# Kernel tuning notes

Hardware: AMD Instinct MI355X
Metric: run time of the kernel (lower is better)

Reference implementation:

```python
import jax, jax.numpy as jnp
import numpy as np

B, S, DIM = 2, 2048, 1024
H, W = 16, 256
HD = DIM // H
SCALE = HD ** -0.5


def setup_inputs() -> dict:
    key = jax.random.key(0)
    ks = jax.random.split(key, 9)
    std = DIM ** -0.5
    return {
        "x": jax.random.normal(ks[0], (B, S, DIM), dtype=jnp.float32),
        "Wq": jax.random.normal(ks[1], (DIM, DIM), dtype=jnp.float32) * std,
        "bq": jnp.zeros((DIM,), dtype=jnp.float32),
        "Wk": jax.random.normal(ks[2], (DIM, DIM), dtype=jnp.float32) * std,
        "bk": jnp.zeros((DIM,), dtype=jnp.float32),
        "Wv": jax.random.normal(ks[3], (DIM, DIM), dtype=jnp.float32) * std,
        "bv": jnp.zeros((DIM,), dtype=jnp.float32),
        "Wo": jax.random.normal(ks[4], (DIM, DIM), dtype=jnp.float32) * std,
        "bo": jnp.zeros((DIM,), dtype=jnp.float32),
    }


def reference(x, Wq, bq, Wk, bk, Wv, bv, Wo, bo):
    b, s, dim = x.shape
    q = (x @ Wq + bq).reshape(b, s, H, HD).transpose(0, 2, 1, 3)  # [B,H,S,HD]
    k = (x @ Wk + bk).reshape(b, s, H, HD).transpose(0, 2, 1, 3)
    v = (x @ Wv + bv).reshape(b, s, H, HD).transpose(0, 2, 1, 3)

    scores = jnp.einsum("bhid,bhjd->bhij", q, k) * SCALE  # [B,H,S,S]
    i = jnp.arange(s)[:, None]
    j = jnp.arange(s)[None, :]
    # valid keys: within causal sliding window [i-W+1, i]
    valid = (j <= i) & (j >= i - W + 1)
    scores = jnp.where(valid, scores, -jnp.inf)
    attn = jax.nn.softmax(scores, axis=-1)
    out = jnp.einsum("bhij,bhjd->bhid", attn, v)  # [B,H,S,HD]
    out = out.transpose(0, 2, 1, 3).reshape(b, s, dim)
    return out @ Wo + bo
```

## Files before the change

### kernel.cpp

```cpp
#include <hip/hip_runtime.h>
#include <stdint.h>

typedef __bf16 bf16;
typedef __bf16 bf16x8 __attribute__((ext_vector_type(8)));
typedef float f32x4 __attribute__((ext_vector_type(4)));

#define MFMA16(a, b, c) __builtin_amdgcn_mfma_f32_16x16x32_bf16((a), (b), (c), 0, 0, 0)

__device__ __forceinline__ void ldsdma16(const void* g, void* l) {
  __builtin_amdgcn_global_load_lds((const __attribute__((address_space(1))) void*)g,
                                   (__attribute__((address_space(3))) void*)l, 16, 0, 0);
}

__global__ __launch_bounds__(256) void prep_kernel(const float* __restrict__ x,
                                                   const float* __restrict__ Wq,
                                                   const float* __restrict__ Wk,
                                                   const float* __restrict__ Wv,
                                                   const float* __restrict__ Wo,
                                                   bf16* __restrict__ WT,
                                                   bf16* __restrict__ xb) {
  if (blockIdx.z == 4) {
    const int t = (blockIdx.y * 16 + blockIdx.x) * 256 + threadIdx.x;
#pragma unroll
    for (int it = 0; it < 16; ++it) {
      const int idx = (it * 65536 + t) * 4;
      float4 v = *(const float4*)(x + idx);
      union { bf16 h[4]; uint2 u; } p;
      p.h[0] = (bf16)v.x; p.h[1] = (bf16)v.y; p.h[2] = (bf16)v.z; p.h[3] = (bf16)v.w;
      *(uint2*)(xb + idx) = p.u;
    }
    return;
  }
  __shared__ float tile[64][65];
  const float* src = blockIdx.z == 0 ? Wq : blockIdx.z == 1 ? Wk : blockIdx.z == 2 ? Wv : Wo;
  bf16* dst = WT + (size_t)blockIdx.z * 1024 * 1024;
  const int k0 = blockIdx.y * 64, n0 = blockIdx.x * 64;
  const int rr = threadIdx.x >> 6, c = threadIdx.x & 63;
#pragma unroll
  for (int i = 0; i < 16; ++i) {
    int r = i * 4 + rr;
    tile[r][c] = src[(size_t)(k0 + r) * 1024 + n0 + c];
  }
  __syncthreads();
#pragma unroll
  for (int i = 0; i < 16; ++i) {
    int r = i * 4 + rr;
    dst[(size_t)(n0 + r) * 1024 + k0 + c] = (bf16)tile[c][r];
  }
}

__global__ __launch_bounds__(256) void qkv_gemm(const bf16* __restrict__ xb,
                                                const bf16* __restrict__ WT,
                                                const float* __restrict__ bq,
                                                const float* __restrict__ bk,
                                                const float* __restrict__ bv,
                                                bf16* __restrict__ QKVc) {
  __shared__ bf16 As[128 * 64] __attribute__((aligned(16)));
  __shared__ bf16 Bs[128 * 64] __attribute__((aligned(16)));
  const int tid = threadIdx.x, lane = tid & 63, wave = tid >> 6;
  const int wm = wave >> 1, wn = wave & 1;
  const int quad = lane >> 4, l16 = lane & 15;
  const int m0 = blockIdx.y * 128, n0 = blockIdx.x * 128;

  f32x4 acc[4][4];
  const f32x4 zero = {0.f, 0.f, 0.f, 0.f};
#pragma unroll
  for (int i = 0; i < 4; ++i)
#pragma unroll
    for (int j = 0; j < 4; ++j) acc[i][j] = zero;

  for (int k0 = 0; k0 < 1024; k0 += 64) {
#pragma unroll
    for (int b2 = 0; b2 < 4; ++b2) {
      int chunk = wave * 256 + b2 * 64 + lane;
      int row = chunk >> 3;
      int cg = (chunk & 7) ^ (row & 7);
      ldsdma16(xb + (size_t)(m0 + row) * 1024 + k0 + cg * 8,
               (char*)As + (size_t)(wave * 256 + b2 * 64) * 16);
      ldsdma16(WT + (size_t)(n0 + row) * 1024 + k0 + cg * 8,
               (char*)Bs + (size_t)(wave * 256 + b2 * 64) * 16);
    }
    __syncthreads();
#pragma unroll
    for (int s = 0; s < 2; ++s) {
      bf16x8 af[4], bfv[4];
#pragma unroll
      for (int i = 0; i < 4; ++i) {
        int ra = wm * 64 + i * 16 + l16;
        af[i] = ((const bf16x8*)As)[ra * 8 + ((s * 4 + quad) ^ (ra & 7))];
        int rb = wn * 64 + i * 16 + l16;
        bfv[i] = ((const bf16x8*)Bs)[rb * 8 + ((s * 4 + quad) ^ (rb & 7))];
      }
#pragma unroll
      for (int i = 0; i < 4; ++i)
#pragma unroll
        for (int j = 0; j < 4; ++j) acc[i][j] = MFMA16(af[i], bfv[j], acc[i][j]);
    }
    __syncthreads();
  }

  const int sel = blockIdx.x >> 3;
  const float* bp = sel == 0 ? bq : sel == 1 ? bk : bv;
  const float scl = (sel == 0) ? 0.18033688f : 1.f;
#pragma unroll
  for (int j = 0; j < 4; ++j) {
    const int n = n0 + wn * 64 + j * 16 + l16;
    const float bias = bp[n & 1023];
#pragma unroll
    for (int i = 0; i < 4; ++i) {
#pragma unroll
      for (int r = 0; r < 4; ++r) {
        const int token = m0 + wm * 64 + i * 16 + quad * 4 + r;
        QKVc[(size_t)token * 3072 + n] = (bf16)((acc[i][j][r] + bias) * scl);
      }
    }
  }
}

__global__ __launch_bounds__(256) void v_transpose(const bf16* __restrict__ QKVc,
                                                   bf16* __restrict__ Vt) {
  __shared__ bf16 tile[64][72] __attribute__((aligned(16)));
  const int tid = threadIdx.x;
  const int st = blockIdx.x, h = blockIdx.y, b = blockIdx.z;
  {
    const int t = tid >> 2, cg = (tid & 3) * 16;
    const bf16* src = QKVc + ((size_t)(b * 2048 + st * 64 + t)) * 3072 + 2048 + h * 64 + cg;
    bf16x8 v0 = *(const bf16x8*)src;
    bf16x8 v1 = *(const bf16x8*)(src + 8);
    *(bf16x8*)&tile[t][cg] = v0;
    *(bf16x8*)&tile[t][cg + 8] = v1;
  }
  __syncthreads();
  const int hd = tid & 63, sg = (tid >> 6) * 16;
  bf16 o[16];
#pragma unroll
  for (int i = 0; i < 16; ++i) o[i] = tile[sg + i][hd];
  bf16* dst = Vt + ((size_t)((b * 16 + h) * 64 + hd)) * 2048 + st * 64 + sg;
  *(bf16x8*)dst = *(bf16x8*)&o[0];
  *(bf16x8*)(dst + 8) = *(bf16x8*)&o[8];
}

__global__ __launch_bounds__(256) void attn_kernel(const bf16* __restrict__ QKVc,
                                                   const bf16* __restrict__ VtG,
                                                   bf16* __restrict__ Ao) {
  __shared__ bf16 Qs[128 * 64] __attribute__((aligned(16)));
  __shared__ bf16 Ks[2][64 * 64] __attribute__((aligned(16)));
  __shared__ bf16 Vs[2][64 * 64] __attribute__((aligned(16)));
  __shared__ bf16 Ps[4][2][16 * 72] __attribute__((aligned(16)));

  const int tid = threadIdx.x, lane = tid & 63, wave = tid >> 6;
  const int quad = lane >> 4, l16 = lane & 15;
  const int qt = blockIdx.x, h = blockIdx.y, b = blockIdx.z;
  const int q0 = qt * 128;
  const size_t vbase = (size_t)(b * 16 + h) * 131072;

#pragma unroll
  for (int inst = 0; inst < 4; ++inst) {
    int d = inst * 256 + wave * 64 + lane;
    int row = d >> 3, cc = d & 7;
    ldsdma16(QKVc + (size_t)(b * 2048 + q0 + row) * 3072 + h * 64 + ((cc ^ (row & 7)) * 8),
             (char*)Qs + (size_t)(inst * 256 + wave * 64) * 16);
  }

  const int lo = (qt >= 2) ? (2 * qt - 4) : 0;
  const int hi = 2 * qt + 1;

  auto stage_kv = [&](int ck, int bu) {
    const int c0k = ck * 64;
#pragma unroll
    for (int inst = 0; inst < 2; ++inst) {
      int d = inst * 256 + wave * 64 + lane;
      int row = d >> 3, cc = d & 7;
      int sc = (cc ^ (row & 7)) * 8;
      ldsdma16(QKVc + (size_t)(b * 2048 + c0k + row) * 3072 + 1024 + h * 64 + sc,
               (char*)Ks[bu] + (size_t)(inst * 256 + wave * 64) * 16);
      ldsdma16(VtG + vbase + (size_t)row * 2048 + c0k + sc,
               (char*)Vs[bu] + (size_t)(inst * 256 + wave * 64) * 16);
    }
  };

  stage_kv(lo, lo & 1);
  __syncthreads();

  bf16x8 qa[2][2];
#pragma unroll
  for (int rt = 0; rt < 2; ++rt) {
    int row = wave * 32 + rt * 16 + l16;
#pragma unroll
    for (int s = 0; s < 2; ++s)
      qa[rt][s] = ((const bf16x8*)Qs)[row * 8 + ((s * 4 + quad) ^ (row & 7))];
  }

  float lrow[2][4];
  f32x4 oacc[2][4];
  const f32x4 zero = {0.f, 0.f, 0.f, 0.f};
#pragma unroll
  for (int rt = 0; rt < 2; ++rt)
#pragma unroll
    for (int r = 0; r < 4; ++r) { lrow[rt][r] = 0.f; oacc[rt][r] = zero; }

  for (int ck = lo; ck <= hi; ++ck) {
    if (ck > lo) __syncthreads();
    if (ck < hi) stage_kv(ck + 1, (ck + 1) & 1);
    const int bu = ck & 1;
    const int c0 = ck * 64;

    bf16x8 kb[4][2], vb[4][2];
#pragma unroll
    for (int nt = 0; nt < 4; ++nt) {
      int rr = nt * 16 + l16;
#pragma unroll
      for (int s = 0; s < 2; ++s) {
        kb[nt][s] = ((const bf16x8*)Ks[bu])[rr * 8 + ((s * 4 + quad) ^ (rr & 7))];
        vb[nt][s] = ((const bf16x8*)Vs[bu])[rr * 8 + ((s * 4 + quad) ^ (rr & 7))];
      }
    }

#pragma unroll
    for (int rt = 0; rt < 2; ++rt) {
      f32x4 sc4[4];
#pragma unroll
      for (int nt = 0; nt < 4; ++nt) {
        f32x4 s = MFMA16(qa[rt][0], kb[nt][0], zero);
        sc4[nt] = MFMA16(qa[rt][1], kb[nt][1], s);
      }

      if (ck >= 2 * qt) {
#pragma unroll
        for (int r = 0; r < 4; ++r) {
          const int i = q0 + wave * 32 + rt * 16 + quad * 4 + r;
#pragma unroll
          for (int nt = 0; nt < 4; ++nt) {
            const int j = c0 + nt * 16 + l16;
            const float p = (j <= i) ? exp2f(sc4[nt][r]) : 0.f;
            sc4[nt][r] = p;
            lrow[rt][r] += p;
          }
        }
      } else if (ck <= 2 * qt - 3) {
#pragma unroll
        for (int r = 0; r < 4; ++r) {
          const int i = q0 + wave * 32 + rt * 16 + quad * 4 + r;
#pragma unroll
          for (int nt = 0; nt < 4; ++nt) {
            const int j = c0 + nt * 16 + l16;
            const float p = (j + 255 >= i) ? exp2f(sc4[nt][r]) : 0.f;
            sc4[nt][r] = p;
            lrow[rt][r] += p;
          }
        }
      } else {
#pragma unroll
        for (int r = 0; r < 4; ++r) {
#pragma unroll
          for (int nt = 0; nt < 4; ++nt) {
            const float p = exp2f(sc4[nt][r]);
            sc4[nt][r] = p;
            lrow[rt][r] += p;
          }
        }
      }

#pragma unroll
      for (int nt = 0; nt < 4; ++nt)
#pragma unroll
        for (int r = 0; r < 4; ++r)
          Ps[wave][rt][(quad * 4 + r) * 72 + nt * 16 + l16] = (bf16)sc4[nt][r];
      asm volatile("s_waitcnt lgkmcnt(0)" ::: "memory");
      bf16x8 pa0 = ((const bf16x8*)Ps[wave][rt])[l16 * 9 + quad];
      bf16x8 pa1 = ((const bf16x8*)Ps[wave][rt])[l16 * 9 + 4 + quad];

#pragma unroll
      for (int ht = 0; ht < 4; ++ht) {
        f32x4 o = MFMA16(pa0, vb[ht][0], oacc[rt][ht]);
        oacc[rt][ht] = MFMA16(pa1, vb[ht][1], o);
      }
    }
  }

#pragma unroll
  for (int rt = 0; rt < 2; ++rt) {
#pragma unroll
    for (int r = 0; r < 4; ++r) {
      float lr = lrow[rt][r];
#pragma unroll
      for (int m = 8; m >= 1; m >>= 1) lr += __shfl_xor(lr, m, 64);
      const float inv = 1.f / lr;
      const int row = q0 + wave * 32 + rt * 16 + quad * 4 + r;
      const size_t outb = ((size_t)(b * 2048 + row)) * 1024 + h * 64;
#pragma unroll
      for (int ht = 0; ht < 4; ++ht)
        Ao[outb + ht * 16 + l16] = (bf16)(oacc[rt][ht][r] * inv);
    }
  }
}

__global__ __launch_bounds__(256) void out_gemm(const bf16* __restrict__ Ain,
                                                const bf16* __restrict__ WoT,
                                                const float* __restrict__ bo,
                                                float* __restrict__ out) {
  __shared__ bf16 As[128 * 64] __attribute__((aligned(16)));
  __shared__ bf16 Bs[64 * 64] __attribute__((aligned(16)));
  const int tid = threadIdx.x, lane = tid & 63, wave = tid >> 6;
  const int wm = wave >> 1, wn = wave & 1;
  const int quad = lane >> 4, l16 = lane & 15;
  const int m0 = blockIdx.y * 128, n0 = blockIdx.x * 64;

  f32x4 acc[4][2];
  const f32x4 zero = {0.f, 0.f, 0.f, 0.f};
#pragma unroll
  for (int i = 0; i < 4; ++i)
#pragma unroll
    for (int j = 0; j < 2; ++j) acc[i][j] = zero;

  for (int k0 = 0; k0 < 1024; k0 += 64) {
#pragma unroll
    for (int b2 = 0; b2 < 4; ++b2) {
      int chunk = wave * 256 + b2 * 64 + lane;
      int row = chunk >> 3;
      int cg = (chunk & 7) ^ (row & 7);
      ldsdma16(Ain + (size_t)(m0 + row) * 1024 + k0 + cg * 8,
               (char*)As + (size_t)(wave * 256 + b2 * 64) * 16);
    }
#pragma unroll
    for (int b2 = 0; b2 < 2; ++b2) {
      int chunk = wave * 128 + b2 * 64 + lane;
      int row = chunk >> 3;
      int cg = (chunk & 7) ^ (row & 7);
      ldsdma16(WoT + (size_t)(n0 + row) * 1024 + k0 + cg * 8,
               (char*)Bs + (size_t)(wave * 128 + b2 * 64) * 16);
    }
    __syncthreads();
#pragma unroll
    for (int s = 0; s < 2; ++s) {
      bf16x8 af[4], bfv[2];
#pragma unroll
      for (int i = 0; i < 4; ++i) {
        int ra = wm * 64 + i * 16 + l16;
        af[i] = ((const bf16x8*)As)[ra * 8 + ((s * 4 + quad) ^ (ra & 7))];
      }
#pragma unroll
      for (int j = 0; j < 2; ++j) {
        int rb = wn * 32 + j * 16 + l16;
        bfv[j] = ((const bf16x8*)Bs)[rb * 8 + ((s * 4 + quad) ^ (rb & 7))];
      }
#pragma unroll
      for (int i = 0; i < 4; ++i)
#pragma unroll
        for (int j = 0; j < 2; ++j) acc[i][j] = MFMA16(af[i], bfv[j], acc[i][j]);
    }
    __syncthreads();
  }

#pragma unroll
  for (int j = 0; j < 2; ++j) {
    const int n = n0 + wn * 32 + j * 16 + l16;
    const float bias = bo[n];
#pragma unroll
    for (int i = 0; i < 4; ++i) {
#pragma unroll
      for (int r = 0; r < 4; ++r) {
        const int token = m0 + wm * 64 + i * 16 + quad * 4 + r;
        out[(size_t)token * 1024 + n] = acc[i][j][r] + bias;
      }
    }
  }
}

extern "C" void kernel_launch(void* const* d_in, const int* in_sizes, int n_in,
                              void* d_out, int out_size, void* d_ws, size_t ws_size,
                              hipStream_t stream) {
  const float* x  = (const float*)d_in[0];
  const float* Wq = (const float*)d_in[1];
  const float* bq = (const float*)d_in[2];
  const float* Wk = (const float*)d_in[3];
  const float* bk = (const float*)d_in[4];
  const float* Wv = (const float*)d_in[5];
  const float* bv = (const float*)d_in[6];
  const float* Wo = (const float*)d_in[7];
  const float* bo = (const float*)d_in[8];
  float* out = (float*)d_out;

  char* ws = (char*)d_ws;
  bf16* xb   = (bf16*)(ws);
  bf16* WT   = (bf16*)(ws + ((size_t)8 << 20));
  bf16* QKVc = (bf16*)(ws + ((size_t)16 << 20));
  bf16* Vt   = (bf16*)(ws + ((size_t)40 << 20));
  bf16* Ao   = (bf16*)(ws + ((size_t)48 << 20));

  prep_kernel<<<dim3(16, 16, 5), 256, 0, stream>>>(x, Wq, Wk, Wv, Wo, WT, xb);
  qkv_gemm<<<dim3(24, 32), 256, 0, stream>>>(xb, WT, bq, bk, bv, QKVc);
  v_transpose<<<dim3(32, 16, 2), 256, 0, stream>>>(QKVc, Vt);
  attn_kernel<<<dim3(16, 16, 2), 256, 0, stream>>>(QKVc, Vt, Ao);
  out_gemm<<<dim3(16, 32), 256, 0, stream>>>(Ao, WT + (size_t)3 * 1024 * 1024, bo, out);
}
```

Baseline: 176.1 us.

## Double-buffer LDS tiles with K=32 stages in QKV and output GEMMs

Both projection GEMMs now use two LDS buffers with a K-step of 32 instead of a single buffer with a K-step of 64. Each iteration starts the global-to-LDS DMA for the next K slice before running the MFMAs on the current one, using one barrier per step instead of two. The swizzle is rewritten for 4-chunk rows. The goal is to hide global load latency behind matrix math, at the cost of twice as many loop iterations and barriers, and less MFMA work between them.

```diff
diff --git a/kernel.cpp b/kernel.cpp
--- a/kernel.cpp
+++ b/kernel.cpp
@@ -55,8 +55,8 @@
                                                 const float* __restrict__ bk,
                                                 const float* __restrict__ bv,
                                                 bf16* __restrict__ QKVc) {
-  __shared__ bf16 As[128 * 64] __attribute__((aligned(16)));
-  __shared__ bf16 Bs[128 * 64] __attribute__((aligned(16)));
+  __shared__ bf16 As[2][128 * 32] __attribute__((aligned(16)));
+  __shared__ bf16 Bs[2][128 * 32] __attribute__((aligned(16)));
   const int tid = threadIdx.x, lane = tid & 63, wave = tid >> 6;
   const int wm = wave >> 1, wn = wave & 1;
   const int quad = lane >> 4, l16 = lane & 15;
@@ -69,34 +69,37 @@
 #pragma unroll
     for (int j = 0; j < 4; ++j) acc[i][j] = zero;
 
-  for (int k0 = 0; k0 < 1024; k0 += 64) {
-#pragma unroll
-    for (int b2 = 0; b2 < 4; ++b2) {
-      int chunk = wave * 256 + b2 * 64 + lane;
-      int row = chunk >> 3;
-      int cg = (chunk & 7) ^ (row & 7);
+  auto stage = [&](int kk, int bu) {
+    const int k0 = kk * 32;
+#pragma unroll
+    for (int inst = 0; inst < 2; ++inst) {
+      int chunk = inst * 256 + tid;
+      int row = chunk >> 2;
+      int cg = (chunk & 3) ^ ((row >> 1) & 3);
       ldsdma16(xb + (size_t)(m0 + row) * 1024 + k0 + cg * 8,
-               (char*)As + (size_t)(wave * 256 + b2 * 64) * 16);
+               (char*)As[bu] + (size_t)(inst * 256 + tid) * 16);
       ldsdma16(WT + (size_t)(n0 + row) * 1024 + k0 + cg * 8,
-               (char*)Bs + (size_t)(wave * 256 + b2 * 64) * 16);
-    }
+               (char*)Bs[bu] + (size_t)(inst * 256 + tid) * 16);
+    }
+  };
+
+  stage(0, 0);
+  for (int k = 0; k < 32; ++k) {
+    const int bu = k & 1;
     __syncthreads();
-#pragma unroll
-    for (int s = 0; s < 2; ++s) {
-      bf16x8 af[4], bfv[4];
-#pragma unroll
-      for (int i = 0; i < 4; ++i) {
-        int ra = wm * 64 + i * 16 + l16;
-        af[i] = ((const bf16x8*)As)[ra * 8 + ((s * 4 + quad) ^ (ra & 7))];
-        int rb = wn * 64 + i * 16 + l16;
-        bfv[i] = ((const bf16x8*)Bs)[rb * 8 + ((s * 4 + quad) ^ (rb & 7))];
-      }
-#pragma unroll
-      for (int i = 0; i < 4; ++i)
-#pragma unroll
-        for (int j = 0; j < 4; ++j) acc[i][j] = MFMA16(af[i], bfv[j], acc[i][j]);
-    }
-    __syncthreads();
+    if (k < 31) stage(k + 1, bu ^ 1);
+    bf16x8 af[4], bfv[4];
+#pragma unroll
+    for (int i = 0; i < 4; ++i) {
+      int ra = wm * 64 + i * 16 + l16;
+      af[i] = ((const bf16x8*)As[bu])[ra * 4 + (quad ^ ((ra >> 1) & 3))];
+      int rb = wn * 64 + i * 16 + l16;
+      bfv[i] = ((const bf16x8*)Bs[bu])[rb * 4 + (quad ^ ((rb >> 1) & 3))];
+    }
+#pragma unroll
+    for (int i = 0; i < 4; ++i)
+#pragma unroll
+      for (int j = 0; j < 4; ++j) acc[i][j] = MFMA16(af[i], bfv[j], acc[i][j]);
   }
 
   const int sel = blockIdx.x >> 3;
@@ -299,8 +302,8 @@
                                                 const bf16* __restrict__ WoT,
                                                 const float* __restrict__ bo,
                                                 float* __restrict__ out) {
-  __shared__ bf16 As[128 * 64] __attribute__((aligned(16)));
-  __shared__ bf16 Bs[64 * 64] __attribute__((aligned(16)));
+  __shared__ bf16 As[2][128 * 32] __attribute__((aligned(16)));
+  __shared__ bf16 Bs[2][64 * 32] __attribute__((aligned(16)));
   const int tid = threadIdx.x, lane = tid & 63, wave = tid >> 6;
   const int wm = wave >> 1, wn = wave & 1;
   const int quad = lane >> 4, l16 = lane & 15;
@@ -313,43 +316,45 @@
 #pragma unroll
     for (int j = 0; j < 2; ++j) acc[i][j] = zero;
 
-  for (int k0 = 0; k0 < 1024; k0 += 64) {
-#pragma unroll
-    for (int b2 = 0; b2 < 4; ++b2) {
-      int chunk = wave * 256 + b2 * 64 + lane;
-      int row = chunk >> 3;
-      int cg = (chunk & 7) ^ (row & 7);
+  auto stage = [&](int kk, int bu) {
+    const int k0 = kk * 32;
+#pragma unroll
+    for (int inst = 0; inst < 2; ++inst) {
+      int chunk = inst * 256 + tid;
+      int row = chunk >> 2;
+      int cg = (chunk & 3) ^ ((row >> 1) & 3);
       ldsdma16(Ain + (size_t)(m0 + row) * 1024 + k0 + cg * 8,
-               (char*)As + (size_t)(wave * 256 + b2 * 64) * 16);
-    }
-#pragma unroll
-    for (int b2 = 0; b2 < 2; ++b2) {
-      int chunk = wave * 128 + b2 * 64 + lane;
-      int row = chunk >> 3;
-      int cg = (chunk & 7) ^ (row & 7);
+               (char*)As[bu] + (size_t)(inst * 256 + tid) * 16);
+    }
+    {
+      int chunk = tid;
+      int row = chunk >> 2;
+      int cg = (chunk & 3) ^ ((row >> 1) & 3);
       ldsdma16(WoT + (size_t)(n0 + row) * 1024 + k0 + cg * 8,
-               (char*)Bs + (size_t)(wave * 128 + b2 * 64) * 16);
-    }
+               (char*)Bs[bu] + (size_t)tid * 16);
+    }
+  };
+
+  stage(0, 0);
+  for (int k = 0; k < 32; ++k) {
+    const int bu = k & 1;
     __syncthreads();
-#pragma unroll
-    for (int s = 0; s < 2; ++s) {
-      bf16x8 af[4], bfv[2];
-#pragma unroll
-      for (int i = 0; i < 4; ++i) {
-        int ra = wm * 64 + i * 16 + l16;
-        af[i] = ((const bf16x8*)As)[ra * 8 + ((s * 4 + quad) ^ (ra & 7))];
-      }
-#pragma unroll
-      for (int j = 0; j < 2; ++j) {
-        int rb = wn * 32 + j * 16 + l16;
-        bfv[j] = ((const bf16x8*)Bs)[rb * 8 + ((s * 4 + quad) ^ (rb & 7))];
-      }
-#pragma unroll
-      for (int i = 0; i < 4; ++i)
-#pragma unroll
-        for (int j = 0; j < 2; ++j) acc[i][j] = MFMA16(af[i], bfv[j], acc[i][j]);
-    }
-    __syncthreads();
+    if (k < 31) stage(k + 1, bu ^ 1);
+    bf16x8 af[4], bfv[2];
+#pragma unroll
+    for (int i = 0; i < 4; ++i) {
+      int ra = wm * 64 + i * 16 + l16;
+      af[i] = ((const bf16x8*)As[bu])[ra * 4 + (quad ^ ((ra >> 1) & 3))];
+    }
+#pragma unroll
+    for (int j = 0; j < 2; ++j) {
+      int rb = wn * 32 + j * 16 + l16;
+      bfv[j] = ((const bf16x8*)Bs[bu])[rb * 4 + (quad ^ ((rb >> 1) & 3))];
+    }
+#pragma unroll
+    for (int i = 0; i < 4; ++i)
+#pragma unroll
+      for (int j = 0; j < 2; ++j) acc[i][j] = MFMA16(af[i], bfv[j], acc[i][j]);
   }
 
 #pragma unroll
```

Result: no change. 176.1 us (+0.0%).
